# Kernel optimization log

Measured on AMD Instinct MI355X. Metric: run time of the kernel, lower is better.

The kernel has to match this reference:

```python
import jax, jax.numpy as jnp
import numpy as np

N = 8192
E_DIM = 256
HID = 256
OUT = 128
N_PRED = 2_000_000


def setup_inputs() -> dict:
    key = jax.random.key(0)
    ks = jax.random.split(key, 6)
    node_indices = jnp.arange(N, dtype=jnp.int64) if jax.config.jax_enable_x64 else jnp.arange(N, dtype=jnp.int32)
    attn_matrix = jax.random.normal(ks[0], (N, N), dtype=jnp.float32)
    edge_label_index = jax.random.randint(ks[1], (2, N_PRED), 0, N)
    emb = jax.random.normal(ks[2], (N, E_DIM), dtype=jnp.float32) * 0.05
    W1 = jax.random.normal(ks[3], (E_DIM, HID), dtype=jnp.float32) * (1.0 / np.sqrt(E_DIM))
    b1 = jnp.zeros((HID,), dtype=jnp.float32)
    W2 = jax.random.normal(ks[4], (HID, OUT), dtype=jnp.float32) * (1.0 / np.sqrt(HID))
    b2 = jnp.zeros((OUT,), dtype=jnp.float32)
    return {"node_indices": node_indices, "attn_matrix": attn_matrix,
            "edge_label_index": edge_label_index, "emb": emb,
            "W1": W1, "b1": b1, "W2": W2, "b2": b2}


def reference(node_indices, attn_matrix, edge_label_index, emb, W1, b1, W2, b2):
    # dense_to_sparse of an (almost surely) all-nonzero dense matrix keeps all
    # N^2 edges (incl. diagonal), so no extra self-loops are added by gcn_norm.
    w = jax.nn.relu(attn_matrix)                       # edge weights after F.relu
    deg = w.sum(axis=0)                                # deg[j] = sum_i w[i,j] (scatter on col)
    dis = jnp.where(deg > 0, jax.lax.rsqrt(deg), 0.0)  # deg^{-1/2}, inf -> 0
    a_norm = dis[:, None] * w * dis[None, :]           # norm_ij = d_i^-1/2 w_ij d_j^-1/2

    x = emb[node_indices]                              # embedding lookup [N, E_DIM]
    # GCNConv: aggregate transformed features at target (col): out = A_norm^T @ (x W) + b
    h = jax.nn.relu(a_norm.T @ (x @ W1) + b1)          # [N, HID]
    z = a_norm.T @ (h @ W2) + b2                       # [N, OUT]

    # decode: dot product between endpoint embeddings
    scores = jnp.einsum('ed,ed->e', z[edge_label_index[0]], z[edge_label_index[1]])
    return scores
```

## Files before the change

### kernel.cpp

```cpp
#include <hip/hip_runtime.h>

typedef _Float16 half8  __attribute__((ext_vector_type(8)));
typedef _Float16 half2v __attribute__((ext_vector_type(2)));
typedef float    floatx4 __attribute__((ext_vector_type(4)));
typedef float    f4v     __attribute__((ext_vector_type(4)));

#define NND 8192
#define PA  40

__device__ __forceinline__ int swzk(int m, int k) { return k ^ (((m >> 3) & 3) << 3); }

__global__ __launch_bounds__(256) void k_deg(const float* __restrict__ A, float* __restrict__ deg) {
    int j4 = blockIdx.x * 256 + threadIdx.x;
    const f4v* Ap = (const f4v*)A + (size_t)blockIdx.y * 128 * 2048 + j4;
    f4v s = {0.f, 0.f, 0.f, 0.f};
    #pragma unroll 4
    for (int i = 0; i < 128; ++i) {
        f4v v = Ap[(size_t)i * 2048];
        s[0] += fmaxf(v[0], 0.f); s[1] += fmaxf(v[1], 0.f);
        s[2] += fmaxf(v[2], 0.f); s[3] += fmaxf(v[3], 0.f);
    }
    #pragma unroll
    for (int c = 0; c < 4; ++c) atomicAdd(&deg[4 * j4 + c], s[c]);
}

__global__ __launch_bounds__(256) void k_dis(const float* __restrict__ deg, float* __restrict__ dis) {
    int j = blockIdx.x * 256 + threadIdx.x;
    float d = deg[j];
    dis[j] = d > 0.f ? 1.f / sqrtf(d) : 0.f;
}

template <typename AT>
__global__ __launch_bounds__(256) void k_mm_small(
    const AT* __restrict__ Abase, const int* __restrict__ gather,
    const float* __restrict__ B, int NB,
    _Float16* __restrict__ outT, const float* __restrict__ dis, float out_scale) {

    __shared__ _Float16 As[128 * PA];
    __shared__ _Float16 Bs[64 * PA];

    int t  = threadIdx.x;
    int i0 = blockIdx.x * 128;
    int n0 = blockIdx.y * 64;

    int am = t & 127, akh = t >> 7;
    int row = i0 + am;
    if (gather) row = gather[row];
    const AT* arow = Abase + (size_t)row * 256;

    int tp = t & 15, kp = t >> 4;

    int lane = t & 63, w = t >> 6;
    int wm = w & 1, wn = w >> 1;
    int lm = lane & 15, q = lane >> 4;

    floatx4 acc[4][2];
    #pragma unroll
    for (int a = 0; a < 4; ++a)
        #pragma unroll
        for (int b = 0; b < 2; ++b) acc[a][b] = (floatx4){0.f, 0.f, 0.f, 0.f};

    for (int ks = 0; ks < 8; ++ks) {
        int c0 = ks * 32;

        half8 av[2];
        if constexpr (sizeof(AT) == 4) {
            #pragma unroll
            for (int cc = 0; cc < 2; ++cc) {
                f4v v0 = *(const f4v*)(arow + c0 + akh * 16 + cc * 8);
                f4v v1 = *(const f4v*)(arow + c0 + akh * 16 + cc * 8 + 4);
                half8 hv;
                #pragma unroll
                for (int e = 0; e < 4; ++e) {
                    hv[e]     = (_Float16)(16.f * v0[e]);
                    hv[4 + e] = (_Float16)(16.f * v1[e]);
                }
                av[cc] = hv;
            }
        } else {
            av[0] = *(const half8*)(arow + c0 + akh * 16);
            av[1] = *(const half8*)(arow + c0 + akh * 16 + 8);
        }

        const float* bp = B + (size_t)(c0 + 2 * kp) * NB + n0 + 4 * tp;
        f4v r0 = *(const f4v*)bp;
        f4v r1 = *(const f4v*)(bp + NB);

        __syncthreads();
        #pragma unroll
        for (int cc = 0; cc < 2; ++cc) {
            int k = akh * 16 + cc * 8;
            *(half8*)(&As[am * PA + swzk(am, k)]) = av[cc];
        }
        #pragma unroll
        for (int u = 0; u < 4; ++u) {
            int n = 4 * tp + u;
            half2v p = {(_Float16)r0[u], (_Float16)r1[u]};
            *(half2v*)(&Bs[n * PA + swzk(n, 2 * kp)]) = p;
        }
        __syncthreads();

        half8 af[4], bf[2];
        #pragma unroll
        for (int mt = 0; mt < 4; ++mt) {
            int m = wm * 64 + mt * 16 + lm;
            af[mt] = *(const half8*)(&As[m * PA + swzk(m, q * 8)]);
        }
        #pragma unroll
        for (int nt = 0; nt < 2; ++nt) {
            int n = wn * 32 + nt * 16 + lm;
            bf[nt] = *(const half8*)(&Bs[n * PA + swzk(n, q * 8)]);
        }
        #pragma unroll
        for (int mt = 0; mt < 4; ++mt)
            #pragma unroll
            for (int nt = 0; nt < 2; ++nt)
                acc[mt][nt] = __builtin_amdgcn_mfma_f32_16x16x32_f16(af[mt], bf[nt], acc[mt][nt], 0, 0, 0);
    }

    #pragma unroll
    for (int mt = 0; mt < 4; ++mt) {
        int ib = i0 + wm * 64 + mt * 16 + q * 4;
        #pragma unroll
        for (int nt = 0; nt < 2; ++nt) {
            int n = n0 + wn * 32 + nt * 16 + lm;
            #pragma unroll
            for (int r = 0; r < 4; ++r) {
                float v = acc[mt][nt][r] * dis[ib + r] * out_scale;
                outT[(size_t)n * NND + ib + r] = (_Float16)v;
            }
        }
    }
}

template <int BN>
__global__ __launch_bounds__(256, 2) void k_mm_big(
    const float* __restrict__ W, const _Float16* __restrict__ Bt, float* __restrict__ C) {

    constexpr int NT  = BN / 32;
    constexpr int NBV = (BN == 256) ? 4 : 2;
    __shared__ _Float16 As[128 * PA];
    __shared__ _Float16 Bs[BN * PA];

    int t = threadIdx.x;
    int j0 = blockIdx.x * 128;
    int i_begin = blockIdx.z * 1024;

    int tp = t & 15, kp = t >> 4;

    int lane = t & 63, w = t >> 6;
    int wm = w & 1, wn = w >> 1;
    int lm = lane & 15, q = lane >> 4;

    floatx4 acc[4][NT];
    #pragma unroll
    for (int a = 0; a < 4; ++a)
        #pragma unroll
        for (int b = 0; b < NT; ++b) acc[a][b] = (floatx4){0.f, 0.f, 0.f, 0.f};

    for (int ks = 0; ks < 32; ++ks) {
        int ib = i_begin + ks * 32;

        const float* r0 = W + (size_t)(ib + 2 * kp) * NND + j0 + tp;
        float fa[8], fb[8];
        #pragma unroll
        for (int u = 0; u < 8; ++u) {
            fa[u] = fmaxf(r0[16 * u], 0.f);
            fb[u] = fmaxf(r0[NND + 16 * u], 0.f);
        }

        half8 bv[NBV];
        if constexpr (BN == 256) {
            const _Float16* src = Bt + (size_t)t * NND + ib;
            #pragma unroll
            for (int c = 0; c < 4; ++c) bv[c] = *(const half8*)(src + 8 * c);
        } else {
            int n = t & 127, kh = t >> 7;
            const _Float16* src = Bt + (size_t)n * NND + ib + 16 * kh;
            #pragma unroll
            for (int c = 0; c < 2; ++c) bv[c] = *(const half8*)(src + 8 * c);
        }

        __syncthreads();
        #pragma unroll
        for (int u = 0; u < 8; ++u) {
            int m = tp + 16 * u;
            half2v p = {(_Float16)fa[u], (_Float16)fb[u]};
            *(half2v*)(&As[m * PA + swzk(m, 2 * kp)]) = p;
        }
        if constexpr (BN == 256) {
            #pragma unroll
            for (int c = 0; c < 4; ++c)
                *(half8*)(&Bs[t * PA + swzk(t, 8 * c)]) = bv[c];
        } else {
            int n = t & 127, kh = t >> 7;
            #pragma unroll
            for (int c = 0; c < 2; ++c) {
                int k = 16 * kh + 8 * c;
                *(half8*)(&Bs[n * PA + swzk(n, k)]) = bv[c];
            }
        }
        __syncthreads();

        half8 af[4], bf[NT];
        #pragma unroll
        for (int mt = 0; mt < 4; ++mt) {
            int m = wm * 64 + mt * 16 + lm;
            af[mt] = *(const half8*)(&As[m * PA + swzk(m, q * 8)]);
        }
        #pragma unroll
        for (int nt = 0; nt < NT; ++nt) {
            int n = wn * (BN / 2) + nt * 16 + lm;
            bf[nt] = *(const half8*)(&Bs[n * PA + swzk(n, q * 8)]);
        }
        #pragma unroll
        for (int mt = 0; mt < 4; ++mt)
            #pragma unroll
            for (int nt = 0; nt < NT; ++nt)
                acc[mt][nt] = __builtin_amdgcn_mfma_f32_16x16x32_f16(af[mt], bf[nt], acc[mt][nt], 0, 0, 0);
    }

    #pragma unroll
    for (int mt = 0; mt < 4; ++mt) {
        int rb = j0 + wm * 64 + mt * 16 + q * 4;
        #pragma unroll
        for (int nt = 0; nt < NT; ++nt) {
            int col = wn * (BN / 2) + nt * 16 + lm;
            #pragma unroll
            for (int r = 0; r < 4; ++r)
                atomicAdd(&C[(size_t)(rb + r) * BN + col], acc[mt][nt][r]);
        }
    }
}

template <int NSH, bool RELU>
__global__ __launch_bounds__(256) void k_finalize(const float* __restrict__ C, const float* __restrict__ dis,
                                                  const float* __restrict__ bias, _Float16* __restrict__ out) {
    int idx = blockIdx.x * 256 + threadIdx.x;
    int j = idx >> NSH;
    int n = idx & ((1 << NSH) - 1);
    float v = C[idx] * (1.f / 1024.f) * dis[j] + bias[n];
    if (RELU) v = fmaxf(v, 0.f);
    out[idx] = (_Float16)(v * 64.f);
}

__global__ __launch_bounds__(256) void k_edges(const _Float16* __restrict__ zh, const int* __restrict__ ei,
                                               float* __restrict__ out, int npred) {
    int g = (blockIdx.x * 256 + threadIdx.x) >> 4;
    int l = threadIdx.x & 15;
    if (g >= npred) return;
    int a = ei[g], b = ei[npred + g];
    half8 za = *(const half8*)(zh + (size_t)a * 128 + l * 8);
    half8 zb = *(const half8*)(zh + (size_t)b * 128 + l * 8);
    float s = 0.f;
    #pragma unroll
    for (int e = 0; e < 8; ++e) s += (float)za[e] * (float)zb[e];
    s += __shfl_xor(s, 1);
    s += __shfl_xor(s, 2);
    s += __shfl_xor(s, 4);
    s += __shfl_xor(s, 8);
    if (l == 0) out[g] = s * (1.f / 4096.f);
}

extern "C" void kernel_launch(void* const* d_in, const int* in_sizes, int n_in,
                              void* d_out, int out_size, void* d_ws, size_t ws_size,
                              hipStream_t stream) {
    const int*   nodes = (const int*)d_in[0];
    const float* attn  = (const float*)d_in[1];
    const int*   eidx  = (const int*)d_in[2];
    const float* emb   = (const float*)d_in[3];
    const float* W1    = (const float*)d_in[4];
    const float* b1    = (const float*)d_in[5];
    const float* W2    = (const float*)d_in[6];
    const float* b2    = (const float*)d_in[7];
    float* out = (float*)d_out;
    int npred = in_sizes[2] / 2;

    char* ws = (char*)d_ws;
    float*    deg = (float*)(ws);
    float*    dis = (float*)(ws + 0x8000);
    float*    C1  = (float*)(ws + 0x10000);
    float*    C2  = (float*)(ws + 0x810000);
    _Float16* M1p = (_Float16*)(ws + 0xC10000);
    _Float16* h   = (_Float16*)(ws + 0x1010000);
    _Float16* M2p = (_Float16*)(ws + 0x1410000);
    _Float16* zh  = (_Float16*)(ws + 0x1610000);

    hipMemsetAsync(deg, 0, 8192 * sizeof(float), stream);
    hipMemsetAsync(C1, 0, (size_t)8192 * 256 * sizeof(float), stream);
    hipMemsetAsync(C2, 0, (size_t)8192 * 128 * sizeof(float), stream);

    k_deg<<<dim3(8, 64), 256, 0, stream>>>(attn, deg);
    k_dis<<<32, 256, 0, stream>>>(deg, dis);

    k_mm_small<float><<<dim3(64, 4), 256, 0, stream>>>(emb, nodes, W1, 256, M1p, dis, 64.f);
    k_mm_big<256><<<dim3(64, 1, 8), 256, 0, stream>>>(attn, M1p, C1);
    k_finalize<8, true><<<8192, 256, 0, stream>>>(C1, dis, b1, h);
    k_mm_small<_Float16><<<dim3(64, 2), 256, 0, stream>>>(h, nullptr, W2, 128, M2p, dis, 16.f);
    k_mm_big<128><<<dim3(64, 1, 8), 256, 0, stream>>>(attn, M2p, C2);
    k_finalize<7, false><<<4096, 256, 0, stream>>>(C2, dis, b2, zh);

    k_edges<<<(npred + 15) / 16, 256, 0, stream>>>(zh, eidx, out, npred);
}
```

Measured before the change: 671.6 us.

## Precompute transposed fp16 relu(attn) once and replace atomics with split-K partials

The degree kernel now also applies relu, converts attn to fp16 and writes it transposed through shared memory. Both big GEMMs then read this half-size, k-contiguous copy with vector loads instead of re-reading the fp32 matrix twice with strided scalar loads. The atomicAdd output accumulation is replaced by per-split partial buffers that the finalize kernel sums, which also removes the two large memsets. The cost is an extra 128MB fp16 write and a larger workspace.

```diff
diff --git a/kernel.cpp b/kernel.cpp
--- a/kernel.cpp
+++ b/kernel.cpp
@@ -1,27 +1,64 @@
 #include <hip/hip_runtime.h>
 
 typedef _Float16 half8  __attribute__((ext_vector_type(8)));
+typedef _Float16 half4v __attribute__((ext_vector_type(4)));
 typedef _Float16 half2v __attribute__((ext_vector_type(2)));
 typedef float    floatx4 __attribute__((ext_vector_type(4)));
 typedef float    f4v     __attribute__((ext_vector_type(4)));
 
 #define NND 8192
 #define PA  40
+#define PT  136
 
 __device__ __forceinline__ int swzk(int m, int k) { return k ^ (((m >> 3) & 3) << 3); }
 
-__global__ __launch_bounds__(256) void k_deg(const float* __restrict__ A, float* __restrict__ deg) {
-    int j4 = blockIdx.x * 256 + threadIdx.x;
-    const f4v* Ap = (const f4v*)A + (size_t)blockIdx.y * 128 * 2048 + j4;
+__global__ __launch_bounds__(256) void k_degT(const float* __restrict__ A,
+                                              _Float16* __restrict__ Wh,
+                                              float* __restrict__ deg) {
+    __shared__ _Float16 T[128 * PT];
+    __shared__ float sdeg[8 * 128];
+    int t  = threadIdx.x;
+    int j0 = blockIdx.x * 128, i0 = blockIdx.y * 128;
+    int c = t & 31;
+    int g = t >> 5;
+
     f4v s = {0.f, 0.f, 0.f, 0.f};
-    #pragma unroll 4
-    for (int i = 0; i < 128; ++i) {
-        f4v v = Ap[(size_t)i * 2048];
-        s[0] += fmaxf(v[0], 0.f); s[1] += fmaxf(v[1], 0.f);
-        s[2] += fmaxf(v[2], 0.f); s[3] += fmaxf(v[3], 0.f);
-    }
-    #pragma unroll
-    for (int c = 0; c < 4; ++c) atomicAdd(&deg[4 * j4 + c], s[c]);
+    #pragma unroll
+    for (int p = 0; p < 2; ++p) {
+        int rb = 64 * p + 8 * g;
+        f4v v[8];
+        #pragma unroll
+        for (int rr = 0; rr < 8; ++rr)
+            v[rr] = *(const f4v*)(A + (size_t)(i0 + rb + rr) * NND + j0 + 4 * c);
+        #pragma unroll
+        for (int rr = 0; rr < 8; ++rr)
+            #pragma unroll
+            for (int u = 0; u < 4; ++u) v[rr][u] = fmaxf(v[rr][u], 0.f);
+        #pragma unroll
+        for (int u = 0; u < 4; ++u) {
+            half8 hv;
+            #pragma unroll
+            for (int rr = 0; rr < 8; ++rr) { hv[rr] = (_Float16)v[rr][u]; s[u] += v[rr][u]; }
+            *(half8*)(&T[(4 * c + u) * PT + rb]) = hv;
+        }
+    }
+    *(f4v*)(&sdeg[g * 128 + 4 * c]) = s;
+    __syncthreads();
+
+    if (t < 128) {
+        float d = 0.f;
+        #pragma unroll
+        for (int g2 = 0; g2 < 8; ++g2) d += sdeg[g2 * 128 + t];
+        atomicAdd(&deg[j0 + t], d);
+    }
+
+    #pragma unroll
+    for (int p = 0; p < 8; ++p) {
+        int j  = 16 * p + (t >> 4);
+        int ic = (t & 15) * 8;
+        half8 hv = *(const half8*)(&T[j * PT + ic]);
+        *(half8*)(Wh + (size_t)(j0 + j) * NND + i0 + ic) = hv;
+    }
 }
 
 __global__ __launch_bounds__(256) void k_dis(const float* __restrict__ deg, float* __restrict__ dis) {
@@ -135,19 +172,18 @@
 
 template <int BN>
 __global__ __launch_bounds__(256, 2) void k_mm_big(
-    const float* __restrict__ W, const _Float16* __restrict__ Bt, float* __restrict__ C) {
-
-    constexpr int NT  = BN / 32;
-    constexpr int NBV = (BN == 256) ? 4 : 2;
+    const _Float16* __restrict__ Wh, const _Float16* __restrict__ Bt, float* __restrict__ Cp) {
+
+    constexpr int NT = BN / 32;
     __shared__ _Float16 As[128 * PA];
     __shared__ _Float16 Bs[BN * PA];
 
     int t = threadIdx.x;
     int j0 = blockIdx.x * 128;
     int i_begin = blockIdx.z * 1024;
-
-    int tp = t & 15, kp = t >> 4;
-
+    float* C = Cp + (size_t)blockIdx.z * NND * BN;
+
+    int ar = t & 127, akh = t >> 7;
     int lane = t & 63, w = t >> 6;
     int wm = w & 1, wn = w >> 1;
     int lm = lane & 15, q = lane >> 4;
@@ -161,15 +197,12 @@
     for (int ks = 0; ks < 32; ++ks) {
         int ib = i_begin + ks * 32;
 
-        const float* r0 = W + (size_t)(ib + 2 * kp) * NND + j0 + tp;
-        float fa[8], fb[8];
-        #pragma unroll
-        for (int u = 0; u < 8; ++u) {
-            fa[u] = fmaxf(r0[16 * u], 0.f);
-            fb[u] = fmaxf(r0[NND + 16 * u], 0.f);
-        }
-
-        half8 bv[NBV];
+        const _Float16* asrc = Wh + (size_t)(j0 + ar) * NND + ib + 16 * akh;
+        half8 av[2];
+        av[0] = *(const half8*)(asrc);
+        av[1] = *(const half8*)(asrc + 8);
+
+        half8 bv[(BN == 256) ? 4 : 2];
         if constexpr (BN == 256) {
             const _Float16* src = Bt + (size_t)t * NND + ib;
             #pragma unroll
@@ -183,10 +216,9 @@
 
         __syncthreads();
         #pragma unroll
-        for (int u = 0; u < 8; ++u) {
-            int m = tp + 16 * u;
-            half2v p = {(_Float16)fa[u], (_Float16)fb[u]};
-            *(half2v*)(&As[m * PA + swzk(m, 2 * kp)]) = p;
+        for (int c = 0; c < 2; ++c) {
+            int k = 16 * akh + 8 * c;
+            *(half8*)(&As[ar * PA + swzk(ar, k)]) = av[c];
         }
         if constexpr (BN == 256) {
             #pragma unroll
@@ -228,18 +260,21 @@
             int col = wn * (BN / 2) + nt * 16 + lm;
             #pragma unroll
             for (int r = 0; r < 4; ++r)
-                atomicAdd(&C[(size_t)(rb + r) * BN + col], acc[mt][nt][r]);
+                C[(size_t)(rb + r) * BN + col] = acc[mt][nt][r];
         }
     }
 }
 
 template <int NSH, bool RELU>
-__global__ __launch_bounds__(256) void k_finalize(const float* __restrict__ C, const float* __restrict__ dis,
+__global__ __launch_bounds__(256) void k_finalize(const float* __restrict__ Cp, const float* __restrict__ dis,
                                                   const float* __restrict__ bias, _Float16* __restrict__ out) {
     int idx = blockIdx.x * 256 + threadIdx.x;
+    float v = 0.f;
+    #pragma unroll
+    for (int z = 0; z < 8; ++z) v += Cp[(size_t)z * (NND << NSH) + idx];
     int j = idx >> NSH;
     int n = idx & ((1 << NSH) - 1);
-    float v = C[idx] * (1.f / 1024.f) * dis[j] + bias[n];
+    v = v * (1.f / 1024.f) * dis[j] + bias[n];
     if (RELU) v = fmaxf(v, 0.f);
     out[idx] = (_Float16)(v * 64.f);
 }
@@ -279,26 +314,25 @@
     char* ws = (char*)d_ws;
     float*    deg = (float*)(ws);
     float*    dis = (float*)(ws + 0x8000);
-    float*    C1  = (float*)(ws + 0x10000);
-    float*    C2  = (float*)(ws + 0x810000);
-    _Float16* M1p = (_Float16*)(ws + 0xC10000);
-    _Float16* h   = (_Float16*)(ws + 0x1010000);
-    _Float16* M2p = (_Float16*)(ws + 0x1410000);
-    _Float16* zh  = (_Float16*)(ws + 0x1610000);
+    _Float16* Wh  = (_Float16*)(ws + 0x10000);
+    float*    C1p = (float*)(ws + 0x8010000);
+    float*    C2p = (float*)(ws + 0xC010000);
+    _Float16* M1p = (_Float16*)(ws + 0xE010000);
+    _Float16* h   = (_Float16*)(ws + 0xE410000);
+    _Float16* M2p = (_Float16*)(ws + 0xE810000);
+    _Float16* zh  = (_Float16*)(ws + 0xEA10000);
 
     hipMemsetAsync(deg, 0, 8192 * sizeof(float), stream);
-    hipMemsetAsync(C1, 0, (size_t)8192 * 256 * sizeof(float), stream);
-    hipMemsetAsync(C2, 0, (size_t)8192 * 128 * sizeof(float), stream);
-
-    k_deg<<<dim3(8, 64), 256, 0, stream>>>(attn, deg);
+
+    k_degT<<<dim3(64, 64), 256, 0, stream>>>(attn, Wh, deg);
     k_dis<<<32, 256, 0, stream>>>(deg, dis);
 
     k_mm_small<float><<<dim3(64, 4), 256, 0, stream>>>(emb, nodes, W1, 256, M1p, dis, 64.f);
-    k_mm_big<256><<<dim3(64, 1, 8), 256, 0, stream>>>(attn, M1p, C1);
-    k_finalize<8, true><<<8192, 256, 0, stream>>>(C1, dis, b1, h);
+    k_mm_big<256><<<dim3(64, 1, 8), 256, 0, stream>>>(Wh, M1p, C1p);
+    k_finalize<8, true><<<8192, 256, 0, stream>>>(C1p, dis, b1, h);
     k_mm_small<_Float16><<<dim3(64, 2), 256, 0, stream>>>(h, nullptr, W2, 128, M2p, dis, 16.f);
-    k_mm_big<128><<<dim3(64, 1, 8), 256, 0, stream>>>(attn, M2p, C2);
-    k_finalize<7, false><<<4096, 256, 0, stream>>>(C2, dis, b2, zh);
+    k_mm_big<128><<<dim3(64, 1, 8), 256, 0, stream>>>(Wh, M2p, C2p);
+    k_finalize<7, false><<<4096, 256, 0, stream>>>(C2p, dis, b2, zh);
 
     k_edges<<<(npred + 15) / 16, 256, 0, stream>>>(zh, eidx, out, npred);
 }
```

After: 645.1 us. 3.9% less time.
